# Kernel tuning notes

Measured on AMD Instinct MI355X. Metric: run time of the kernel, lower is better.

Reference implementation:

```python
import jax, jax.numpy as jnp
import numpy as np

N_NODES = 100000
N_EDGES = 600000
D_FEAT = 128
EDIM = 128
N_CLASSES = 10


def setup_inputs() -> dict:
    key = jax.random.key(0)
    k_h, k_eh, k_w, k_b, k_s, k_d = jax.random.split(key, 6)
    h = jax.random.normal(k_h, (N_NODES, D_FEAT), dtype=jnp.float32)
    edge_h = jax.random.normal(k_eh, (N_EDGES, 1, EDIM), dtype=jnp.float32)
    # Linear(in_features*2 + edim -> out_classes); torch stores weight as [out, in]
    W_w = jax.random.normal(k_w, (N_CLASSES, 2 * D_FEAT + EDIM), dtype=jnp.float32) * 0.05
    W_b = jax.random.normal(k_b, (N_CLASSES,), dtype=jnp.float32) * 0.05
    src = jax.random.randint(k_s, (N_EDGES,), 0, N_NODES, dtype=jnp.int64)
    dst = jax.random.randint(k_d, (N_EDGES,), 0, N_NODES, dtype=jnp.int64)
    return {"h": h, "edge_h": edge_h, "W_w": W_w, "W_b": W_b, "src": src, "dst": dst}


def reference(h, edge_h, W_w, W_b, src, dst):
    # edge-wise gather of src/dst node features
    h_u = h[src]                      # [E, D]
    h_v = h[dst]                      # [E, D]
    h_uv = edge_h.reshape(edge_h.shape[0], edge_h.shape[2])  # [E, edim]
    feat = jnp.concatenate([h_u, h_v, h_uv], axis=1)          # [E, 2D+edim]
    score = feat @ W_w.T + W_b                                 # [E, C]
    return score
```

## Files before the change

### kernel.cpp

```cpp
#include <hip/hip_runtime.h>


typedef __attribute__((ext_vector_type(8))) short    short8;
typedef __attribute__((ext_vector_type(4))) float    f32x4;
typedef __attribute__((ext_vector_type(4))) unsigned short us4;

#define NC    10
#define EPW   16
#define ROWUS 392

__device__ __forceinline__ unsigned short f2bf(float f) {
    unsigned u = __builtin_bit_cast(unsigned, f);
    u += 0x7FFFu + ((u >> 16) & 1u);
    return (unsigned short)(u >> 16);
}

__global__ __launch_bounds__(64, 4) void mlp_edge_mfma(
    const float* __restrict__ h,
    const float* __restrict__ eh,
    const float* __restrict__ Ww,
    const float* __restrict__ Wb,
    const int*   __restrict__ src,
    const int*   __restrict__ dst,
    float* __restrict__ out,
    int E)
{
    __shared__ __align__(16) unsigned short lds[EPW * ROWUS];

    const int  l    = threadIdx.x;
    const long base = (long)blockIdx.x * EPW;
    const int  n    = l & 15;
    const int  q    = l >> 4;
    const int  r8   = l & ~0 ? (l >> 3) : 0;
    const int  c8   = l & 7;

    const long eA  = base + (l >> 3);
    const long eB  = base + 8 + (l >> 3);
    const long eAc = (eA < E) ? eA : (long)(E - 1);
    const long eBc = (eB < E) ? eB : (long)(E - 1);
    const int  sA = src[eAc], sB = src[eBc];
    const int  dA = dst[eAc], dB = dst[eBc];

    short8 bf[12];
#pragma unroll
    for (int t = 0; t < 12; ++t) bf[t] = (short8)0;
    if (n < NC) {
        const float* wr = Ww + n * 384 + q * 8;
#pragma unroll
        for (int t = 0; t < 12; ++t) {
            const f32x4 w0 = *(const f32x4*)(wr + t * 32);
            const f32x4 w1 = *(const f32x4*)(wr + t * 32 + 4);
            short8 b;
            b[0] = (short)f2bf(w0[0]); b[1] = (short)f2bf(w0[1]);
            b[2] = (short)f2bf(w0[2]); b[3] = (short)f2bf(w0[3]);
            b[4] = (short)f2bf(w1[0]); b[5] = (short)f2bf(w1[1]);
            b[6] = (short)f2bf(w1[2]); b[7] = (short)f2bf(w1[3]);
            bf[t] = b;
        }
    }

#define STAGE(gaddrA, gaddrB, so) do {                                        \
    _Pragma("unroll")                                                         \
    for (int seg = 0; seg < 4; ++seg) {                                       \
        const f32x4 va = *(const f32x4*)((gaddrA) + seg * 32 + c8 * 4);       \
        const f32x4 vb = *(const f32x4*)((gaddrB) + seg * 32 + c8 * 4);       \
        us4 ua, ub;                                                           \
        ua[0]=f2bf(va[0]); ua[1]=f2bf(va[1]); ua[2]=f2bf(va[2]); ua[3]=f2bf(va[3]); \
        ub[0]=f2bf(vb[0]); ub[1]=f2bf(vb[1]); ub[2]=f2bf(vb[2]); ub[3]=f2bf(vb[3]); \
        *(us4*)&lds[(l >> 3) * ROWUS + (so) + seg * 32 + c8 * 4]       = ua;  \
        *(us4*)&lds[((l >> 3) + 8) * ROWUS + (so) + seg * 32 + c8 * 4] = ub;  \
    } } while (0)

    STAGE(h  + (long)sA * 128, h  + (long)sB * 128, 0);
    STAGE(h  + (long)dA * 128, h  + (long)dB * 128, 128);
    STAGE(eh + eAc * 128,      eh + eBc * 128,      256);
#undef STAGE

    __syncthreads();

    f32x4 acc = {0.f, 0.f, 0.f, 0.f};
    const unsigned short* arow = &lds[n * ROWUS + q * 8];
#pragma unroll
    for (int t = 0; t < 12; ++t) {
        const short8 af = *(const short8*)(arow + t * 32);
        acc = __builtin_amdgcn_mfma_f32_16x16x32_bf16(af, bf[t], acc, 0, 0, 0);
    }

    if (n < NC) {
        const float bias = Wb[n];
#pragma unroll
        for (int r = 0; r < 4; ++r) {
            const long e = base + q * 4 + r;
            if (e < E) out[e * NC + n] = acc[r] + bias;
        }
    }
}

extern "C" void kernel_launch(void* const* d_in, const int* in_sizes, int n_in,
                              void* d_out, int out_size, void* d_ws, size_t ws_size,
                              hipStream_t stream) {
    const float* h   = (const float*)d_in[0];
    const float* eh  = (const float*)d_in[1];
    const float* Ww  = (const float*)d_in[2];
    const float* Wb  = (const float*)d_in[3];
    const int*   src = (const int*)d_in[4];
    const int*   dst = (const int*)d_in[5];
    float* out = (float*)d_out;

    const int E = in_sizes[4];
    const int blocks = (E + EPW - 1) / EPW;
    mlp_edge_mfma<<<blocks, 64, 0, stream>>>(h, eh, Ww, Wb, src, dst, out, E);
}
```

Before: 488.4 us.

## Load gathered rows directly into MFMA fragments, precompute weight fragments, multi-tile blocks

Removes the LDS staging and barrier: each lane now loads its own edge row slices straight into registers in the MFMA A-operand layout and converts them to bf16 in place. Weight fragments are built once by a small pre-kernel into workspace instead of being converted in every block. Each block now processes four 16-edge tiles in a loop, with loads for the next gather group issued before computing the current one. The cost is higher register pressure (launch bounds lowered to 3) and one extra kernel launch.

```diff
diff --git a/kernel.cpp b/kernel.cpp
--- a/kernel.cpp
+++ b/kernel.cpp
@@ -1,13 +1,12 @@
 #include <hip/hip_runtime.h>
 
 
-typedef __attribute__((ext_vector_type(8))) short    short8;
-typedef __attribute__((ext_vector_type(4))) float    f32x4;
-typedef __attribute__((ext_vector_type(4))) unsigned short us4;
+typedef __attribute__((ext_vector_type(8))) short short8;
+typedef __attribute__((ext_vector_type(4))) float f32x4;
 
-#define NC    10
-#define EPW   16
-#define ROWUS 392
+#define NC   10
+#define TPW  4
+#define NFRAG 12
 
 __device__ __forceinline__ unsigned short f2bf(float f) {
     unsigned u = __builtin_bit_cast(unsigned, f);
@@ -15,83 +14,97 @@
     return (unsigned short)(u >> 16);
 }
 
-__global__ __launch_bounds__(64, 4) void mlp_edge_mfma(
+__device__ __forceinline__ short8 cvt8(f32x4 a, f32x4 b) {
+    short8 s;
+    s[0]=(short)f2bf(a[0]); s[1]=(short)f2bf(a[1]);
+    s[2]=(short)f2bf(a[2]); s[3]=(short)f2bf(a[3]);
+    s[4]=(short)f2bf(b[0]); s[5]=(short)f2bf(b[1]);
+    s[6]=(short)f2bf(b[2]); s[7]=(short)f2bf(b[3]);
+    return s;
+}
+
+__global__ void build_wfrag(const float* __restrict__ Ww, short8* __restrict__ frag) {
+    const int l = threadIdx.x;
+    const int n = l & 15;
+    const int q = l >> 4;
+#pragma unroll
+    for (int t = 0; t < NFRAG; ++t) {
+        short8 b = (short8)0;
+        if (n < NC) {
+            const float* w = Ww + n * 384 + t * 32 + q * 8;
+            const f32x4 w0 = *(const f32x4*)(w);
+            const f32x4 w1 = *(const f32x4*)(w + 4);
+            b = cvt8(w0, w1);
+        }
+        frag[t * 64 + l] = b;
+    }
+}
+
+#define LG(v0,v1,v2,v3,v4,v5,v6,v7,p)           \
+    v0 = *(const f32x4*)((p) + 0);              \
+    v1 = *(const f32x4*)((p) + 4);              \
+    v2 = *(const f32x4*)((p) + 32);             \
+    v3 = *(const f32x4*)((p) + 36);             \
+    v4 = *(const f32x4*)((p) + 64);             \
+    v5 = *(const f32x4*)((p) + 68);             \
+    v6 = *(const f32x4*)((p) + 96);             \
+    v7 = *(const f32x4*)((p) + 100);
+
+#define CG(g, v0,v1,v2,v3,v4,v5,v6,v7)                                        \
+    acc = __builtin_amdgcn_mfma_f32_16x16x32_bf16(cvt8(v0,v1), bf[(g)*4+0], acc, 0,0,0); \
+    acc = __builtin_amdgcn_mfma_f32_16x16x32_bf16(cvt8(v2,v3), bf[(g)*4+1], acc, 0,0,0); \
+    acc = __builtin_amdgcn_mfma_f32_16x16x32_bf16(cvt8(v4,v5), bf[(g)*4+2], acc, 0,0,0); \
+    acc = __builtin_amdgcn_mfma_f32_16x16x32_bf16(cvt8(v6,v7), bf[(g)*4+3], acc, 0,0,0);
+
+__global__ __launch_bounds__(64, 3) void mlp_edge_mfma(
     const float* __restrict__ h,
     const float* __restrict__ eh,
-    const float* __restrict__ Ww,
+    const short8* __restrict__ frag,
     const float* __restrict__ Wb,
     const int*   __restrict__ src,
     const int*   __restrict__ dst,
     float* __restrict__ out,
     int E)
 {
-    __shared__ __align__(16) unsigned short lds[EPW * ROWUS];
+    const int l = threadIdx.x;
+    const int n = l & 15;
+    const int q = l >> 4;
 
-    const int  l    = threadIdx.x;
-    const long base = (long)blockIdx.x * EPW;
-    const int  n    = l & 15;
-    const int  q    = l >> 4;
-    const int  r8   = l & ~0 ? (l >> 3) : 0;
-    const int  c8   = l & 7;
+    short8 bf[NFRAG];
+#pragma unroll
+    for (int t = 0; t < NFRAG; ++t) bf[t] = frag[t * 64 + l];
+    const float bias = (n < NC) ? Wb[n] : 0.f;
 
-    const long eA  = base + (l >> 3);
-    const long eB  = base + 8 + (l >> 3);
-    const long eAc = (eA < E) ? eA : (long)(E - 1);
-    const long eBc = (eB < E) ? eB : (long)(E - 1);
-    const int  sA = src[eAc], sB = src[eBc];
-    const int  dA = dst[eAc], dB = dst[eBc];
+    const long tile0 = (long)blockIdx.x * TPW;
 
-    short8 bf[12];
+#pragma unroll 1
+    for (int tt = 0; tt < TPW; ++tt) {
+        const long base = (tile0 + tt) * 16;
+        if (base >= E) break;
+        const long e  = base + n;
+        const long ec = (e < E) ? e : (long)(E - 1);
+        const float* ps = h  + (long)src[ec] * 128 + q * 8;
+        const float* pd = h  + (long)dst[ec] * 128 + q * 8;
+        const float* pe = eh + ec * 128 + q * 8;
+
+        f32x4 x0,x1,x2,x3,x4,x5,x6,x7;
+        f32x4 y0,y1,y2,y3,y4,y5,y6,y7;
+
+        f32x4 acc = {0.f, 0.f, 0.f, 0.f};
+
+        LG(x0,x1,x2,x3,x4,x5,x6,x7, ps)
+        LG(y0,y1,y2,y3,y4,y5,y6,y7, pd)
+        CG(0, x0,x1,x2,x3,x4,x5,x6,x7)
+        LG(x0,x1,x2,x3,x4,x5,x6,x7, pe)
+        CG(1, y0,y1,y2,y3,y4,y5,y6,y7)
+        CG(2, x0,x1,x2,x3,x4,x5,x6,x7)
+
+        if (n < NC) {
 #pragma unroll
-    for (int t = 0; t < 12; ++t) bf[t] = (short8)0;
-    if (n < NC) {
-        const float* wr = Ww + n * 384 + q * 8;
-#pragma unroll
-        for (int t = 0; t < 12; ++t) {
-            const f32x4 w0 = *(const f32x4*)(wr + t * 32);
-            const f32x4 w1 = *(const f32x4*)(wr + t * 32 + 4);
-            short8 b;
-            b[0] = (short)f2bf(w0[0]); b[1] = (short)f2bf(w0[1]);
-            b[2] = (short)f2bf(w0[2]); b[3] = (short)f2bf(w0[3]);
-            b[4] = (short)f2bf(w1[0]); b[5] = (short)f2bf(w1[1]);
-            b[6] = (short)f2bf(w1[2]); b[7] = (short)f2bf(w1[3]);
-            bf[t] = b;
-        }
-    }
-
-#define STAGE(gaddrA, gaddrB, so) do {                                        \
-    _Pragma("unroll")                                                         \
-    for (int seg = 0; seg < 4; ++seg) {                                       \
-        const f32x4 va = *(const f32x4*)((gaddrA) + seg * 32 + c8 * 4);       \
-        const f32x4 vb = *(const f32x4*)((gaddrB) + seg * 32 + c8 * 4);       \
-        us4 ua, ub;                                                           \
-        ua[0]=f2bf(va[0]); ua[1]=f2bf(va[1]); ua[2]=f2bf(va[2]); ua[3]=f2bf(va[3]); \
-        ub[0]=f2bf(vb[0]); ub[1]=f2bf(vb[1]); ub[2]=f2bf(vb[2]); ub[3]=f2bf(vb[3]); \
-        *(us4*)&lds[(l >> 3) * ROWUS + (so) + seg * 32 + c8 * 4]       = ua;  \
-        *(us4*)&lds[((l >> 3) + 8) * ROWUS + (so) + seg * 32 + c8 * 4] = ub;  \
-    } } while (0)
-
-    STAGE(h  + (long)sA * 128, h  + (long)sB * 128, 0);
-    STAGE(h  + (long)dA * 128, h  + (long)dB * 128, 128);
-    STAGE(eh + eAc * 128,      eh + eBc * 128,      256);
-#undef STAGE
-
-    __syncthreads();
-
-    f32x4 acc = {0.f, 0.f, 0.f, 0.f};
-    const unsigned short* arow = &lds[n * ROWUS + q * 8];
-#pragma unroll
-    for (int t = 0; t < 12; ++t) {
-        const short8 af = *(const short8*)(arow + t * 32);
-        acc = __builtin_amdgcn_mfma_f32_16x16x32_bf16(af, bf[t], acc, 0, 0, 0);
-    }
-
-    if (n < NC) {
-        const float bias = Wb[n];
-#pragma unroll
-        for (int r = 0; r < 4; ++r) {
-            const long e = base + q * 4 + r;
-            if (e < E) out[e * NC + n] = acc[r] + bias;
+            for (int r = 0; r < 4; ++r) {
+                const long e2 = base + q * 4 + r;
+                if (e2 < E) out[e2 * NC + n] = acc[r] + bias;
+            }
         }
     }
 }
@@ -108,6 +121,11 @@
     float* out = (float*)d_out;
 
     const int E = in_sizes[4];
-    const int blocks = (E + EPW - 1) / EPW;
-    mlp_edge_mfma<<<blocks, 64, 0, stream>>>(h, eh, Ww, Wb, src, dst, out, E);
+    short8* frag = (short8*)d_ws;
+
+    build_wfrag<<<1, 64, 0, stream>>>(Ww, frag);
+
+    const int edgesPerBlock = 16 * TPW;
+    const int blocks = (E + edgesPerBlock - 1) / edgesPerBlock;
+    mlp_edge_mfma<<<blocks, 64, 0, stream>>>(h, eh, frag, Wb, src, dst, out, E);
 }
```

Measured after the change: 495.3 us. Within noise of the previous version (+1.4%).
